# Kernel optimization log

Hardware: AMD Instinct MI355X
Metric: run time of the kernel (lower is better)

Reference implementation:

```python
import jax, jax.numpy as jnp
import numpy as np
from jax import lax

DIM = 64
HEADS = 2
BATCH, H, W = 4, 192, 192


def _conv1x1(x, w, b=None):
    # x: [b,c,h,w], w: [o,c]
    y = jnp.einsum('bchw,oc->bohw', x, w)
    if b is not None:
        y = y + b[None, :, None, None]
    return y


def _gelu(x):
    return jax.nn.gelu(x, approximate=False)  # torch nn.GELU default (erf)


def setup_inputs() -> dict:
    key = jax.random.key(0)
    ks = jax.random.split(key, 25)
    C = DIM
    n = lambda k, s, scale=0.05: jax.random.normal(k, s, dtype=jnp.float32) * scale
    return {
        'x': jax.random.normal(ks[0], (BATCH, C, H, W), dtype=jnp.float32),
        # BSConvU: pointwise (no bias) + depthwise 3x3 (bias)
        'pw_w': n(ks[1], (C, C)),
        'dw_w': n(ks[2], (C, 1, 3, 3)),
        'dw_b': n(ks[3], (C,)),
        'conv2_w': n(ks[4], (C, C)), 'conv2_b': n(ks[5], (C,)),
        'conv0_w': n(ks[6], (C, C)), 'conv0_b': n(ks[7], (C,)),
        # SelfAttention (bias=False)
        'att_q_w': n(ks[8], (C, C)), 'att_k_w': n(ks[9], (C, C)),
        'att_v_w': n(ks[10], (C, C)), 'att_proj_w': n(ks[11], (C, C)),
        'temperature': jnp.ones((HEADS, 1, 1), dtype=jnp.float32),
        # RowAttention (bias=False)
        'row_q_w': n(ks[12], (C, C)), 'row_k_w': n(ks[13], (C, C)),
        'row_v_w': n(ks[14], (C, C)),
        'row_gamma': n(ks[15], (1,), 0.5),
        # ColAttention (bias=False)
        'col_q_w': n(ks[16], (C, C)), 'col_k_w': n(ks[17], (C, C)),
        'col_v_w': n(ks[18], (C, C)),
        'col_gamma': n(ks[19], (1,), 0.5),
        # final fuse conv: in=3C, out=C
        'conv_w': n(ks[20], (C, 3 * C)), 'conv_b': n(ks[21], (C,)),
    }


def reference(x, pw_w, dw_w, dw_b, conv2_w, conv2_b, conv0_w, conv0_b,
              att_q_w, att_k_w, att_v_w, att_proj_w, temperature,
              row_q_w, row_k_w, row_v_w, row_gamma,
              col_q_w, col_k_w, col_v_w, col_gamma,
              conv_w, conv_b):
    b, c, h, w = x.shape
    # --- BSConvU -> GELU -> conv_2, plus conv_0 skip ---
    t = _conv1x1(x, pw_w)
    t = lax.conv_general_dilated(
        t, dw_w, window_strides=(1, 1), padding=((1, 1), (1, 1)),
        feature_group_count=c,
        dimension_numbers=('NCHW', 'OIHW', 'NCHW')) + dw_b[None, :, None, None]
    x1 = _conv1x1(_gelu(t), conv2_w, conv2_b) + _conv1x1(x, conv0_w, conv0_b)

    # --- channel self-attention (out_1) ---
    ch = c // HEADS
    q = _conv1x1(x1, att_q_w).reshape(b, HEADS, ch, h * w)
    k = _conv1x1(x1, att_k_w).reshape(b, HEADS, ch, h * w)
    v = _conv1x1(x1, att_v_w).reshape(b, HEADS, ch, h * w)
    q = q / jnp.maximum(jnp.linalg.norm(q, axis=-1, keepdims=True), 1e-12)
    k = k / jnp.maximum(jnp.linalg.norm(k, axis=-1, keepdims=True), 1e-12)
    attn = jnp.einsum('bgcn,bgdn->bgcd', q, k) * temperature[None]
    attn = jax.nn.softmax(attn, axis=-1)
    out1 = jnp.einsum('bgcd,bgdn->bgcn', attn, v).reshape(b, c, h, w)
    out1 = _conv1x1(out1, att_proj_w)

    # --- row attention over width, per (batch,row) (out_2) ---
    Q = _conv1x1(x1, row_q_w)
    K = _conv1x1(x1, row_k_w)
    V = _conv1x1(out1, row_v_w)
    s = jnp.einsum('bchi,bchj->bhij', Q, K)         # [b,h,w,w]
    a = jax.nn.softmax(s, axis=-1)
    out2 = jnp.einsum('bchj,bhij->bchi', V, a)
    out2 = row_gamma * out2 + x1

    # --- col attention over height, per (batch,col) (out_3) ---
    Q = _conv1x1(x1, col_q_w)
    K = _conv1x1(x1, col_k_w)
    V = _conv1x1(out1, col_v_w)
    s = jnp.einsum('bciw,bcjw->bwij', Q, K)         # [b,w,h,h]
    a = jax.nn.softmax(s, axis=-1)
    out3 = jnp.einsum('bcjw,bwij->bciw', V, a)
    out3 = col_gamma * out3 + x1

    out = jnp.concatenate([out1, out2, out3], axis=1)
    return _gelu(_conv1x1(out, conv_w, conv_b))
```

## Files before the change

kernel.cpp:

```cpp
#include <hip/hip_runtime.h>
#include <hip/hip_fp16.h>
#include <cstdio>

#define BB 4
#define C 64
#define HH 192
#define WW 192
#define NPIX (HH*WW)
#define ST (BB*C*NPIX)

__device__ __forceinline__ float gelu_f(float v) {
    return 0.5f * v * (1.0f + erff(v * 0.70710678118654752440f));
}

template<bool TWO_IN, bool PERB, bool DO_GELU>
__global__ __launch_bounds__(256, 3) void k_gconv(
    const float* __restrict__ in1, const float* __restrict__ in2,
    const float* __restrict__ W1, const float* __restrict__ W2,
    const float* __restrict__ bias1, const float* __restrict__ bias2,
    float* __restrict__ out, int ldw1, int ldw2)
{
    extern __shared__ float sm[];
    float* Wl = sm;
    float* Xl = sm + 4352;
    const int t = threadIdx.x;
    const int px0 = blockIdx.x * 128;
    const int b = blockIdx.y;
    const size_t base = (size_t)b*(C*NPIX) + px0;
    const int to = t >> 5, tp = t & 31;
    const int o0 = to*8, p0 = tp*4;
    float acc[8][4];
#pragma unroll
    for (int k = 0; k < 8; ++k) {
        float bo = 0.f;
        if (bias1) bo += bias1[o0+k];
        if (bias2) bo += bias2[o0+k];
#pragma unroll
        for (int m = 0; m < 4; ++m) acc[k][m] = bo;
    }
    const int NIN = TWO_IN ? 2 : 1;
#pragma unroll
    for (int inp = 0; inp < NIN; ++inp) {
        const float* In = inp ? in2 : in1;
        const float* Wk = inp ? W2 : (PERB ? W1 + b*4096 : W1);
        const int ldw = inp ? ldw2 : ldw1;
#pragma unroll
        for (int k = 0; k < 16; ++k) {
            const int idx = k*256 + t;
            const int o = idx >> 6, c = idx & 63;
            Wl[c*68 + o] = Wk[o*ldw + c];
        }
#pragma unroll
        for (int k = 0; k < 8; ++k) {
            const int f4 = k*256 + t;
            const int c = f4 >> 5, p4 = (f4 & 31)*4;
            *reinterpret_cast<float4*>(&Xl[c*132 + p4]) =
                *reinterpret_cast<const float4*>(&In[base + (size_t)c*NPIX + p4]);
        }
        __syncthreads();
#pragma unroll 2
        for (int c = 0; c < 64; ++c) {
            const float4 wa = *reinterpret_cast<const float4*>(&Wl[c*68 + o0]);
            const float4 wb = *reinterpret_cast<const float4*>(&Wl[c*68 + o0 + 4]);
            const float4 xv = *reinterpret_cast<const float4*>(&Xl[c*132 + p0]);
            const float wr[8] = {wa.x,wa.y,wa.z,wa.w, wb.x,wb.y,wb.z,wb.w};
            const float xr[4] = {xv.x,xv.y,xv.z,xv.w};
#pragma unroll
            for (int k = 0; k < 8; ++k)
#pragma unroll
                for (int m = 0; m < 4; ++m) acc[k][m] += wr[k]*xr[m];
        }
        __syncthreads();
    }
#pragma unroll
    for (int k = 0; k < 8; ++k) {
        float4 o4;
        if (DO_GELU) {
            o4.x = gelu_f(acc[k][0]); o4.y = gelu_f(acc[k][1]);
            o4.z = gelu_f(acc[k][2]); o4.w = gelu_f(acc[k][3]);
        } else {
            o4.x = acc[k][0]; o4.y = acc[k][1];
            o4.z = acc[k][2]; o4.w = acc[k][3];
        }
        *reinterpret_cast<float4*>(&out[base + (size_t)(o0+k)*NPIX + p0]) = o4;
    }
}

__global__ __launch_bounds__(256, 3) void k_conv4(
    const float* __restrict__ i1, const float* __restrict__ i2,
    const float* __restrict__ i3, const float* __restrict__ i4,
    const float* __restrict__ W1, const float* __restrict__ W2,
    const float* __restrict__ W3, const float* __restrict__ W4,
    const float* __restrict__ bias, float* __restrict__ out)
{
    extern __shared__ float sm[];
    float* Wl = sm;
    float* Xl = sm + 4352;
    const int t = threadIdx.x;
    const int px0 = blockIdx.x * 128;
    const int b = blockIdx.y;
    const size_t base = (size_t)b*(C*NPIX) + px0;
    const int to = t >> 5, tp = t & 31;
    const int o0 = to*8, p0 = tp*4;
    float acc[8][4];
#pragma unroll
    for (int k = 0; k < 8; ++k) {
        const float bo = bias[o0+k];
#pragma unroll
        for (int m = 0; m < 4; ++m) acc[k][m] = bo;
    }
#pragma unroll
    for (int inp = 0; inp < 4; ++inp) {
        const float* In = (inp==0)?i1:(inp==1)?i2:(inp==2)?i3:i4;
        const float* Wk = (inp==0)?W1:(inp==1)?W2:(inp==2)?W3:W4;
        const int ldw = (inp==0)?192:64;
#pragma unroll
        for (int k = 0; k < 16; ++k) {
            const int idx = k*256 + t;
            const int o = idx >> 6, c = idx & 63;
            Wl[c*68 + o] = Wk[o*ldw + c];
        }
#pragma unroll
        for (int k = 0; k < 8; ++k) {
            const int f4 = k*256 + t;
            const int c = f4 >> 5, p4 = (f4 & 31)*4;
            *reinterpret_cast<float4*>(&Xl[c*132 + p4]) =
                *reinterpret_cast<const float4*>(&In[base + (size_t)c*NPIX + p4]);
        }
        __syncthreads();
#pragma unroll 2
        for (int c = 0; c < 64; ++c) {
            const float4 wa = *reinterpret_cast<const float4*>(&Wl[c*68 + o0]);
            const float4 wb = *reinterpret_cast<const float4*>(&Wl[c*68 + o0 + 4]);
            const float4 xv = *reinterpret_cast<const float4*>(&Xl[c*132 + p0]);
            const float wr[8] = {wa.x,wa.y,wa.z,wa.w, wb.x,wb.y,wb.z,wb.w};
            const float xr[4] = {xv.x,xv.y,xv.z,xv.w};
#pragma unroll
            for (int k = 0; k < 8; ++k)
#pragma unroll
                for (int m = 0; m < 4; ++m) acc[k][m] += wr[k]*xr[m];
        }
        __syncthreads();
    }
#pragma unroll
    for (int k = 0; k < 8; ++k) {
        float4 o4;
        o4.x = gelu_f(acc[k][0]); o4.y = gelu_f(acc[k][1]);
        o4.z = gelu_f(acc[k][2]); o4.w = gelu_f(acc[k][3]);
        *reinterpret_cast<float4*>(&out[base + (size_t)(o0+k)*NPIX + p0]) = o4;
    }
}

__global__ __launch_bounds__(192) void k_dw(
    const float* __restrict__ t0, const float* __restrict__ w,
    const float* __restrict__ bias, float* __restrict__ g)
{
    const int x = threadIdx.x;
    const int y = blockIdx.x;
    const int bc = blockIdx.y;
    const int c = bc & 63;
    const float* img = t0 + bc * NPIX;
    const float* wc = w + c * 9;
    float acc = bias[c];
#pragma unroll
    for (int dy = -1; dy <= 1; ++dy) {
        const int yy = y + dy;
        if (yy < 0 || yy > 191) continue;
#pragma unroll
        for (int dx = -1; dx <= 1; ++dx) {
            const int xx = x + dx;
            if (xx < 0 || xx > 191) continue;
            acc += img[yy*WW + xx] * wc[(dy+1)*3 + (dx+1)];
        }
    }
    g[bc*NPIX + y*WW + x] = gelu_f(acc);
}

__global__ __launch_bounds__(256) void k_gram_part(
    const float* __restrict__ x1p, float* __restrict__ part)
{
    extern __shared__ float lt[];
    const int chunk = blockIdx.x, b = blockIdx.y, t = threadIdx.x;
    const int gbase = b * (C*NPIX) + chunk * 256;
    for (int idx = t; idx < C*256; idx += 256) {
        const int c = idx >> 8, n = idx & 255;
        lt[n*68 + c] = x1p[gbase + c*NPIX + n];
    }
    __syncthreads();
    const int ti = t & 15, tj = t >> 4;
    float acc[4][4];
#pragma unroll
    for (int r = 0; r < 4; ++r)
#pragma unroll
        for (int s = 0; s < 4; ++s) acc[r][s] = 0.f;
    for (int n = 0; n < 256; ++n) {
        const float4 av = *reinterpret_cast<const float4*>(&lt[n*68 + 4*ti]);
        const float4 bv = *reinterpret_cast<const float4*>(&lt[n*68 + 4*tj]);
        const float ar[4] = {av.x, av.y, av.z, av.w};
        const float br[4] = {bv.x, bv.y, bv.z, bv.w};
#pragma unroll
        for (int r = 0; r < 4; ++r)
#pragma unroll
            for (int s = 0; s < 4; ++s) acc[r][s] += ar[r] * br[s];
    }
    float* pb = part + (b*144 + chunk)*4096;
#pragma unroll
    for (int r = 0; r < 4; ++r)
#pragma unroll
        for (int s = 0; s < 4; ++s) pb[(4*ti+r)*64 + (4*tj+s)] = acc[r][s];
}

__global__ __launch_bounds__(256) void k_gram_reduce(
    const float* __restrict__ part, float* __restrict__ G1)
{
    const int flat = blockIdx.x*256 + threadIdx.x;
    const int b = flat >> 12, ij = flat & 4095;
    float s = 0.f;
    for (int ch = 0; ch < 144; ++ch) s += part[(b*144+ch)*4096 + ij];
    G1[flat] = s;
}

__global__ __launch_bounds__(256) void k_attn_small(
    const float* __restrict__ G1a, const float* __restrict__ Wq,
    const float* __restrict__ Wk, const float* __restrict__ Wv,
    const float* __restrict__ Wp, const float* __restrict__ temp,
    float* __restrict__ M2)
{
    extern __shared__ float sm[];
    float* g1 = sm;
    float* wa = sm + 4096;
    float* wb = sm + 8192;
    float* u  = sm + 12288;
    float* at = sm + 16384;
    float* nq = sm + 18432;
    float* nk = sm + 18496;
    const int b = blockIdx.x, t = threadIdx.x;
    const float* G = G1a + b*4096;
    for (int i = t; i < 4096; i += 256) { g1[i] = G[i]; wa[i] = Wq[i]; wb[i] = Wk[i]; }
    __syncthreads();
    {
        const int r = t >> 2, q4 = t & 3;
        for (int cc = q4*16; cc < q4*16 + 16; ++cc) {
            float s = 0.f;
            for (int k = 0; k < 64; ++k) s += wa[r*64+k] * g1[k*64+cc];
            u[r*64+cc] = s;
        }
    }
    __syncthreads();
    {
        const int d = t >> 2, kq = t & 3;
        float p = 0.f;
        for (int k = kq*16; k < kq*16 + 16; ++k) {
            float tk = 0.f;
            for (int c2 = 0; c2 < 64; ++c2) tk += g1[k*64+c2] * wb[d*64+c2];
            p += wb[d*64+k] * tk;
        }
        p += __shfl_xor(p, 1);
        p += __shfl_xor(p, 2);
        if (kq == 0) nk[d] = sqrtf(fmaxf(p, 0.f));
    }
    if (t < 64) {
        float s = 0.f;
        for (int c2 = 0; c2 < 64; ++c2) s += u[t*64+c2] * wa[t*64+c2];
        nq[t] = sqrtf(fmaxf(s, 0.f));
    }
    __syncthreads();
    if (t < 64) {
        const int gI = t >> 5;
        const float tg = temp[gI];
        const float dq = fmaxf(nq[t], 1e-12f);
        float row[32];
        float mx = -1e30f;
#pragma unroll
        for (int d2 = 0; d2 < 32; ++d2) {
            const int dd = gI*32 + d2;
            float s = 0.f;
            for (int c2 = 0; c2 < 64; ++c2) s += u[t*64+c2] * wb[dd*64+c2];
            s = s * tg / (dq * fmaxf(nk[dd], 1e-12f));
            row[d2] = s; mx = fmaxf(mx, s);
        }
        float se = 0.f;
#pragma unroll
        for (int d2 = 0; d2 < 32; ++d2) { row[d2] = __expf(row[d2]-mx); se += row[d2]; }
        const float inv = 1.f / se;
#pragma unroll
        for (int d2 = 0; d2 < 32; ++d2) at[t*32+d2] = row[d2]*inv;
    }
    __syncthreads();
    for (int i = t; i < 4096; i += 256) { wa[i] = Wv[i]; wb[i] = Wp[i]; }
    __syncthreads();
    {
        const int m = t >> 2, q4 = t & 3, gI = m >> 5;
        for (int e = q4*16; e < q4*16 + 16; ++e) {
            float s = 0.f;
#pragma unroll
            for (int d2 = 0; d2 < 32; ++d2) s += at[m*32+d2] * wa[(gI*32+d2)*64 + e];
            g1[m*64+e] = s;
        }
    }
    __syncthreads();
    {
        const int o = t >> 2, q4 = t & 3;
        for (int e = q4*16; e < q4*16 + 16; ++e) {
            float s = 0.f;
            for (int m = 0; m < 64; ++m) s += wb[o*64+m] * g1[m*64+e];
            M2[b*4096 + o*64+e] = s;
        }
    }
}

__global__ __launch_bounds__(256) void k_small_mats(
    const float* __restrict__ rq, const float* __restrict__ rk,
    const float* __restrict__ cq, const float* __restrict__ ck,
    const float* __restrict__ fw, const float* __restrict__ rv,
    const float* __restrict__ cv, const float* __restrict__ rg,
    const float* __restrict__ cg,
    float* __restrict__ Wtr, float* __restrict__ Wtc,
    float* __restrict__ Wf2p, float* __restrict__ Wf3p,
    float* __restrict__ Wfx)
{
    const int which = blockIdx.x, t = threadIdx.x;
    const int a = t >> 2, b0 = (t & 3) * 16;
    if (which <= 1) {
        const float* Q = which ? cq : rq;
        const float* Kw = which ? ck : rk;
        float* O = which ? Wtc : Wtr;
        for (int b = b0; b < b0 + 16; ++b) {
            float s = 0.f;
            for (int co = 0; co < 64; ++co) s += Q[co*64 + a] * Kw[co*64 + b];
            O[a*64 + b] = s;
        }
    } else if (which <= 3) {
        const float* Vw = (which == 2) ? rv : cv;
        const float g = (which == 2) ? rg[0] : cg[0];
        const int off = (which == 2) ? 64 : 128;
        float* O = (which == 2) ? Wf2p : Wf3p;
        for (int b = b0; b < b0 + 16; ++b) {
            float s = 0.f;
            for (int m = 0; m < 64; ++m) s += fw[a*192 + off + m] * Vw[m*64 + b];
            O[a*64 + b] = g * s;
        }
    } else {
        for (int b = b0; b < b0 + 16; ++b)
            Wfx[a*64 + b] = fw[a*192 + 64 + b] + fw[a*192 + 128 + b];
    }
}

#define SP 196
__global__ __launch_bounds__(256, 2) void k_attn_fused(
    const float* __restrict__ X, const float* __restrict__ Wt,
    const float* __restrict__ U, float* __restrict__ Z)
{
    extern __shared__ float sm[];
    float* Xl = sm;
    __half* Ylh = reinterpret_cast<__half*>(sm + 12544);
    __half* Plh = reinterpret_cast<__half*>(sm);
    float* red  = sm;
    float* mrow = sm + 3264;
    float* lrow = sm + 18816;
    const int t = threadIdx.x;
    const int h = blockIdx.x, b = blockIdx.y;
    const size_t gbase = (size_t)b*(C*NPIX) + (size_t)h*WW;

#pragma unroll 4
    for (int k = 0; k < 48; ++k) {
        const int idx = k*256 + t;
        const int c = idx / 192, j = idx - c*192;
        Xl[c*SP + j] = X[gbase + (size_t)c*NPIX + j];
    }
    __syncthreads();

    {
        const int tc = t & 15, tjy = t >> 4;
        const int c0 = 4*tc, j0y = 12*tjy;
        float accy[4][12];
#pragma unroll
        for (int k = 0; k < 4; ++k)
#pragma unroll
            for (int m = 0; m < 12; ++m) accy[k][m] = 0.f;
        for (int a = 0; a < 64; ++a) {
            const float4 w4 = *reinterpret_cast<const float4*>(&Wt[a*64 + c0]);
            const float4 xa = *reinterpret_cast<const float4*>(&Xl[a*SP + j0y]);
            const float4 xb = *reinterpret_cast<const float4*>(&Xl[a*SP + j0y + 4]);
            const float4 xc = *reinterpret_cast<const float4*>(&Xl[a*SP + j0y + 8]);
            const float wr[4]  = {w4.x, w4.y, w4.z, w4.w};
            const float xr[12] = {xa.x,xa.y,xa.z,xa.w, xb.x,xb.y,xb.z,xb.w,
                                  xc.x,xc.y,xc.z,xc.w};
#pragma unroll
            for (int k = 0; k < 4; ++k)
#pragma unroll
                for (int m = 0; m < 12; ++m) accy[k][m] += wr[k] * xr[m];
        }
#pragma unroll
        for (int k = 0; k < 4; ++k) {
            __half2* yr = reinterpret_cast<__half2*>(&Ylh[(c0+k)*SP + j0y]);
#pragma unroll
            for (int q = 0; q < 6; ++q)
                yr[q] = __floats2half2_rn(accy[k][2*q], accy[k][2*q+1]);
        }
    }
    __syncthreads();

    const int ti = t & 15, tj = t >> 4;
    const int i0 = ti*12, j0 = tj*12;
    float acc[12][12];
#pragma unroll
    for (int r = 0; r < 12; ++r)
#pragma unroll
        for (int s = 0; s < 12; ++s) acc[r][s] = 0.f;
#pragma unroll 2
    for (int c = 0; c < 64; ++c) {
        const float4 xa = *reinterpret_cast<const float4*>(&Xl[c*SP + i0]);
        const float4 xb = *reinterpret_cast<const float4*>(&Xl[c*SP + i0 + 4]);
        const float4 xc = *reinterpret_cast<const float4*>(&Xl[c*SP + i0 + 8]);
        const __half2* yp = reinterpret_cast<const __half2*>(&Ylh[c*SP + j0]);
        const float2 y0 = __half22float2(yp[0]);
        const float2 y1 = __half22float2(yp[1]);
        const float2 y2 = __half22float2(yp[2]);
        const float2 y3 = __half22float2(yp[3]);
        const float2 y4 = __half22float2(yp[4]);
        const float2 y5 = __half22float2(yp[5]);
        const float xr[12] = {xa.x,xa.y,xa.z,xa.w, xb.x,xb.y,xb.z,xb.w, xc.x,xc.y,xc.z,xc.w};
        const float yr[12] = {y0.x,y0.y, y1.x,y1.y, y2.x,y2.y,
                              y3.x,y3.y, y4.x,y4.y, y5.x,y5.y};
#pragma unroll
        for (int r = 0; r < 12; ++r)
#pragma unroll
            for (int s = 0; s < 12; ++s) acc[r][s] += xr[r] * yr[s];
    }
    __syncthreads();

#pragma unroll
    for (int r = 0; r < 12; ++r) {
        float pm = acc[r][0];
#pragma unroll
        for (int s = 1; s < 12; ++s) pm = fmaxf(pm, acc[r][s]);
        red[(i0 + r)*17 + tj] = pm;
    }
    __syncthreads();
    if (t < 192) {
        float m = red[t*17];
#pragma unroll
        for (int k = 1; k < 16; ++k) m = fmaxf(m, red[t*17 + k]);
        mrow[t] = m;
    }
    __syncthreads();
#pragma unroll
    for (int r = 0; r < 12; ++r) {
        const float mi = mrow[i0 + r];
        float ps = 0.f;
#pragma unroll
        for (int s = 0; s < 12; ++s) {
            acc[r][s] = __expf(acc[r][s] - mi);
            ps += acc[r][s];
        }
        red[(i0 + r)*17 + tj] = ps;
    }
    __syncthreads();
    if (t < 192) {
        float l = 0.f;
#pragma unroll
        for (int k = 0; k < 16; ++k) l += red[t*17 + k];
        lrow[t] = 1.f / l;
    }
    __syncthreads();

#pragma unroll
    for (int r = 0; r < 12; ++r) {
        __half2* pr = reinterpret_cast<__half2*>(&Plh[(i0 + r)*SP + j0]);
#pragma unroll
        for (int q = 0; q < 6; ++q)
            pr[q] = __floats2half2_rn(acc[r][2*q], acc[r][2*q+1]);
    }
    __syncthreads();

    const int ci = t & 15, ii = t >> 4;
    const int c0z = 4*ci, i0z = 12*ii;
    const float* Ub = U + gbase;
    float accz[4][12];
#pragma unroll
    for (int k = 0; k < 4; ++k)
#pragma unroll
        for (int m = 0; m < 12; ++m) accz[k][m] = 0.f;
#pragma unroll 2
    for (int jq = 0; jq < 48; ++jq) {
        const int j4 = 4*jq;
        float4 u4[4];
#pragma unroll
        for (int k = 0; k < 4; ++k)
            u4[k] = *reinterpret_cast<const float4*>(&Ub[(size_t)(c0z+k)*NPIX + j4]);
        float2 pa[12], pb[12];
#pragma unroll
        for (int m = 0; m < 12; ++m) {
            const __half2* pp = reinterpret_cast<const __half2*>(&Plh[(i0z+m)*SP + j4]);
            pa[m] = __half22float2(pp[0]);
            pb[m] = __half22float2(pp[1]);
        }
#pragma unroll
        for (int k = 0; k < 4; ++k)
#pragma unroll
            for (int m = 0; m < 12; ++m) {
                accz[k][m] += u4[k].x * pa[m].x + u4[k].y * pa[m].y
                            + u4[k].z * pb[m].x + u4[k].w * pb[m].y;
            }
    }
    float lr[12];
#pragma unroll
    for (int m = 0; m < 12; ++m) lr[m] = lrow[i0z + m];
#pragma unroll
    for (int k = 0; k < 4; ++k) {
        float* zr = Z + gbase + (size_t)(c0z + k)*NPIX + i0z;
        float4 o0, o1, o2;
        o0.x = accz[k][0]*lr[0]; o0.y = accz[k][1]*lr[1];  o0.z = accz[k][2]*lr[2];   o0.w = accz[k][3]*lr[3];
        o1.x = accz[k][4]*lr[4]; o1.y = accz[k][5]*lr[5];  o1.z = accz[k][6]*lr[6];   o1.w = accz[k][7]*lr[7];
        o2.x = accz[k][8]*lr[8]; o2.y = accz[k][9]*lr[9];  o2.z = accz[k][10]*lr[10]; o2.w = accz[k][11]*lr[11];
        *reinterpret_cast<float4*>(zr)     = o0;
        *reinterpret_cast<float4*>(zr + 4) = o1;
        *reinterpret_cast<float4*>(zr + 8) = o2;
    }
}

__global__ __launch_bounds__(256) void k_transpose(
    const float* __restrict__ in, float* __restrict__ out)
{
    __shared__ float tile[32][33];
    const int tx = threadIdx.x & 31, ty = threadIdx.x >> 5;
    const int x0 = blockIdx.x*32, y0 = blockIdx.y*32;
    const float* img = in + blockIdx.z * NPIX;
    float* og = out + blockIdx.z * NPIX;
#pragma unroll
    for (int r = ty; r < 32; r += 8) tile[r][tx] = img[(y0+r)*WW + x0+tx];
    __syncthreads();
#pragma unroll
    for (int r = ty; r < 32; r += 8) og[(x0+r)*WW + (y0+tx)] = tile[tx][r];
}

__global__ __launch_bounds__(256) void k_transpose2(
    const float* __restrict__ inA, float* __restrict__ outA,
    const float* __restrict__ inB, float* __restrict__ outB)
{
    __shared__ float tile[32][33];
    const int tx = threadIdx.x & 31, ty = threadIdx.x >> 5;
    const int x0 = blockIdx.x*32, y0 = blockIdx.y*32;
    const int z = blockIdx.z;
    const float* img = (z < BB*C) ? inA + (size_t)z*NPIX
                                  : inB + (size_t)(z - BB*C)*NPIX;
    float* og = (z < BB*C) ? outA + (size_t)z*NPIX
                           : outB + (size_t)(z - BB*C)*NPIX;
#pragma unroll
    for (int r = ty; r < 32; r += 8) tile[r][tx] = img[(y0+r)*WW + x0+tx];
    __syncthreads();
#pragma unroll
    for (int r = ty; r < 32; r += 8) og[(x0+r)*WW + (y0+tx)] = tile[tx][r];
}

extern "C" void kernel_launch(void* const* d_in, const int* in_sizes, int n_in,
                              void* d_out, int out_size, void* d_ws, size_t ws_size,
                              hipStream_t stream) {
    const float* x       = (const float*)d_in[0];
    const float* pw_w    = (const float*)d_in[1];
    const float* dw_w    = (const float*)d_in[2];
    const float* dw_b    = (const float*)d_in[3];
    const float* conv2_w = (const float*)d_in[4];
    const float* conv2_b = (const float*)d_in[5];
    const float* conv0_w = (const float*)d_in[6];
    const float* conv0_b = (const float*)d_in[7];
    const float* attq    = (const float*)d_in[8];
    const float* attk    = (const float*)d_in[9];
    const float* attv    = (const float*)d_in[10];
    const float* attp    = (const float*)d_in[11];
    const float* temp    = (const float*)d_in[12];
    const float* rq      = (const float*)d_in[13];
    const float* rk      = (const float*)d_in[14];
    const float* rv      = (const float*)d_in[15];
    const float* rg      = (const float*)d_in[16];
    const float* cq      = (const float*)d_in[17];
    const float* ck      = (const float*)d_in[18];
    const float* cv      = (const float*)d_in[19];
    const float* cg      = (const float*)d_in[20];
    const float* fw      = (const float*)d_in[21];
    const float* fb      = (const float*)d_in[22];

    float* ws = (float*)d_ws;
    float* A  = ws;
    float* Bf = ws + (size_t)ST;
    float* Cf = ws + 2*(size_t)ST;
    float* Df = ws + 3*(size_t)ST;
    float* Ef = ws + 4*(size_t)ST;
    float* partials = ws + 5*(size_t)ST;
    float* G1 = partials + 576*4096;
    float* M2 = G1 + 16384;
    float* Wtr  = M2 + 16384;
    float* Wtc  = Wtr + 4096;
    float* Wf2p = Wtc + 4096;
    float* Wf3p = Wf2p + 4096;
    float* Wfx  = Wf3p + 4096;

    const size_t need = ((size_t)5*ST + 576*4096 + 16384 + 16384 + 5*4096)
                        * sizeof(float);
    if (ws_size < need) {
        fprintf(stderr, "kernel_launch: ws_size %zu < needed %zu\n", ws_size, need);
        return;
    }

    (void)hipFuncSetAttribute((const void*)k_gram_part,
        hipFuncAttributeMaxDynamicSharedMemorySize, 69632);
    (void)hipFuncSetAttribute((const void*)k_attn_small,
        hipFuncAttributeMaxDynamicSharedMemorySize, 74240);
    (void)hipFuncSetAttribute((const void*)k_attn_fused,
        hipFuncAttributeMaxDynamicSharedMemorySize, 76032);
    (void)hipFuncSetAttribute((const void*)k_conv4,
        hipFuncAttributeMaxDynamicSharedMemorySize, 51200);
    (void)hipFuncSetAttribute((const void*)(k_gconv<false,false,false>),
        hipFuncAttributeMaxDynamicSharedMemorySize, 51200);
    (void)hipFuncSetAttribute((const void*)(k_gconv<true,false,false>),
        hipFuncAttributeMaxDynamicSharedMemorySize, 51200);
    (void)hipFuncSetAttribute((const void*)(k_gconv<false,true,false>),
        hipFuncAttributeMaxDynamicSharedMemorySize, 51200);

    const dim3 blk256(256), blk192(192);
    const dim3 gconv(NPIX/128, BB);
    const dim3 ggram(NPIX/256, BB);
    const dim3 gline(HH, BB);
    const dim3 gtr(6, 6, BB*C);
    const dim3 gtr2(6, 6, 2*BB*C);

    k_small_mats<<<dim3(5), blk256, 0, stream>>>(rq, rk, cq, ck, fw, rv, cv,
                                                 rg, cg, Wtr, Wtc, Wf2p, Wf3p, Wfx);
    k_gconv<false,false,false><<<gconv, blk256, 51200, stream>>>(
        x, nullptr, pw_w, nullptr, nullptr, nullptr, A, 64, 64);
    k_dw<<<dim3(HH, BB*C), blk192, 0, stream>>>(A, dw_w, dw_b, Bf);
    k_gconv<true,false,false><<<gconv, blk256, 51200, stream>>>(
        Bf, x, conv2_w, conv0_w, conv2_b, conv0_b, A, 64, 64);
    k_gram_part<<<ggram, blk256, 69632, stream>>>(A, partials);
    k_gram_reduce<<<dim3(64), blk256, 0, stream>>>(partials, G1);
    k_attn_small<<<dim3(BB), blk256, 74240, stream>>>(G1, attq, attk, attv, attp, temp, M2);
    k_gconv<false,true,false><<<gconv, blk256, 51200, stream>>>(
        A, nullptr, M2, nullptr, nullptr, nullptr, Bf, 64, 64);
    k_transpose2<<<gtr2, blk256, 0, stream>>>(A, Cf, Bf, Df);
    k_attn_fused<<<gline, blk256, 76032, stream>>>(Cf, Wtc, Df, Ef);
    k_transpose<<<gtr, blk256, 0, stream>>>(Ef, Df);
    k_attn_fused<<<gline, blk256, 76032, stream>>>(A, Wtr, Bf, Cf);
    k_conv4<<<gconv, blk256, 51200, stream>>>(
        Bf, Cf, Df, A, fw, Wf2p, Wf3p, Wfx, fb, (float*)d_out);
}
```

Before: 841.2 us.

## Use packed fp16 dot2 instructions in fused row/column attention matmuls

Stores X, Y, P and U as packed half2 with channel pairs interleaved, and replaces the scalar fp32 FMA inner loops of the three attention matmuls with v_dot2 fp16 accumulate-to-fp32 instructions. Each dot2 does two multiply-adds, so the ALU work in the Q·K score, projection and P·V stages should roughly halve, and shared-memory footprint per element shrinks. In exchange, X, the projection weights and V are now rounded to fp16 with round-toward-zero conversion (previously X and V stayed fp32), which lowers accuracy, and the layout change increases shared memory slightly.

```diff
diff --git a/kernel.cpp b/kernel.cpp
--- a/kernel.cpp
+++ b/kernel.cpp
@@ -1,5 +1,4 @@
 #include <hip/hip_runtime.h>
-#include <hip/hip_fp16.h>
 #include <cstdio>
 
 #define BB 4
@@ -11,6 +10,32 @@
 
 __device__ __forceinline__ float gelu_f(float v) {
     return 0.5f * v * (1.0f + erff(v * 0.70710678118654752440f));
+}
+
+typedef __fp16 h2 __attribute__((ext_vector_type(2)));
+
+__device__ __forceinline__ h2 pkh2(float lo, float hi) {
+#if __has_builtin(__builtin_amdgcn_cvt_pkrtz)
+    return __builtin_amdgcn_cvt_pkrtz(lo, hi);
+#else
+    h2 r; r[0] = (__fp16)lo; r[1] = (__fp16)hi; return r;
+#endif
+}
+
+__device__ __forceinline__ float dot2f(h2 a, h2 b, float c) {
+#if __has_builtin(__builtin_amdgcn_fdot2)
+    return __builtin_amdgcn_fdot2(a, b, c, false);
+#else
+    return c + (float)a[0]*(float)b[0] + (float)a[1]*(float)b[1];
+#endif
+}
+
+__device__ __forceinline__ void ld4h2(const void* p, h2* d) {
+    const float4 f = *reinterpret_cast<const float4*>(p);
+    d[0] = __builtin_bit_cast(h2, f.x);
+    d[1] = __builtin_bit_cast(h2, f.y);
+    d[2] = __builtin_bit_cast(h2, f.z);
+    d[3] = __builtin_bit_cast(h2, f.w);
 }
 
 template<bool TWO_IN, bool PERB, bool DO_GELU>
@@ -347,26 +372,29 @@
 }
 
 #define SP 196
+#define PSTR 100
 __global__ __launch_bounds__(256, 2) void k_attn_fused(
     const float* __restrict__ X, const float* __restrict__ Wt,
     const float* __restrict__ U, float* __restrict__ Z)
 {
     extern __shared__ float sm[];
-    float* Xl = sm;
-    __half* Ylh = reinterpret_cast<__half*>(sm + 12544);
-    __half* Plh = reinterpret_cast<__half*>(sm);
+    h2* Xh = reinterpret_cast<h2*>(sm);
+    h2* Yh = reinterpret_cast<h2*>(sm + 6272);
+    h2* Ph = reinterpret_cast<h2*>(sm);
     float* red  = sm;
     float* mrow = sm + 3264;
-    float* lrow = sm + 18816;
+    float* lrow = sm + 19200;
     const int t = threadIdx.x;
     const int h = blockIdx.x, b = blockIdx.y;
     const size_t gbase = (size_t)b*(C*NPIX) + (size_t)h*WW;
 
 #pragma unroll 4
-    for (int k = 0; k < 48; ++k) {
+    for (int k = 0; k < 24; ++k) {
         const int idx = k*256 + t;
-        const int c = idx / 192, j = idx - c*192;
-        Xl[c*SP + j] = X[gbase + (size_t)c*NPIX + j];
+        const int cc = idx / 192, j = idx - cc*192;
+        const float lo = X[gbase + (size_t)(2*cc)*NPIX + j];
+        const float hi = X[gbase + (size_t)(2*cc+1)*NPIX + j];
+        Xh[cc*SP + j] = pkh2(lo, hi);
     }
     __syncthreads();
 
@@ -378,25 +406,26 @@
         for (int k = 0; k < 4; ++k)
 #pragma unroll
             for (int m = 0; m < 12; ++m) accy[k][m] = 0.f;
-        for (int a = 0; a < 64; ++a) {
-            const float4 w4 = *reinterpret_cast<const float4*>(&Wt[a*64 + c0]);
-            const float4 xa = *reinterpret_cast<const float4*>(&Xl[a*SP + j0y]);
-            const float4 xb = *reinterpret_cast<const float4*>(&Xl[a*SP + j0y + 4]);
-            const float4 xc = *reinterpret_cast<const float4*>(&Xl[a*SP + j0y + 8]);
-            const float wr[4]  = {w4.x, w4.y, w4.z, w4.w};
-            const float xr[12] = {xa.x,xa.y,xa.z,xa.w, xb.x,xb.y,xb.z,xb.w,
-                                  xc.x,xc.y,xc.z,xc.w};
+        for (int aa = 0; aa < 32; ++aa) {
+            const float4 wlo = *reinterpret_cast<const float4*>(&Wt[(2*aa)*64 + c0]);
+            const float4 whi = *reinterpret_cast<const float4*>(&Wt[(2*aa+1)*64 + c0]);
+            h2 wh[4];
+            wh[0] = pkh2(wlo.x, whi.x); wh[1] = pkh2(wlo.y, whi.y);
+            wh[2] = pkh2(wlo.z, whi.z); wh[3] = pkh2(wlo.w, whi.w);
+            h2 xh[12];
+            ld4h2(&Xh[aa*SP + j0y],     xh);
+            ld4h2(&Xh[aa*SP + j0y + 4], xh+4);
+            ld4h2(&Xh[aa*SP + j0y + 8], xh+8);
 #pragma unroll
             for (int k = 0; k < 4; ++k)
 #pragma unroll
-                for (int m = 0; m < 12; ++m) accy[k][m] += wr[k] * xr[m];
-        }
-#pragma unroll
-        for (int k = 0; k < 4; ++k) {
-            __half2* yr = reinterpret_cast<__half2*>(&Ylh[(c0+k)*SP + j0y]);
-#pragma unroll
-            for (int q = 0; q < 6; ++q)
-                yr[q] = __floats2half2_rn(accy[k][2*q], accy[k][2*q+1]);
+                for (int m = 0; m < 12; ++m)
+                    accy[k][m] = dot2f(wh[k], xh[m], accy[k][m]);
+        }
+#pragma unroll
+        for (int m = 0; m < 12; ++m) {
+            Yh[(2*tc)*SP + j0y + m]   = pkh2(accy[0][m], accy[1][m]);
+            Yh[(2*tc+1)*SP + j0y + m] = pkh2(accy[2][m], accy[3][m]);
         }
     }
     __syncthreads();
@@ -409,24 +438,19 @@
 #pragma unroll
         for (int s = 0; s < 12; ++s) acc[r][s] = 0.f;
 #pragma unroll 2
-    for (int c = 0; c < 64; ++c) {
-        const float4 xa = *reinterpret_cast<const float4*>(&Xl[c*SP + i0]);
-        const float4 xb = *reinterpret_cast<const float4*>(&Xl[c*SP + i0 + 4]);
-        const float4 xc = *reinterpret_cast<const float4*>(&Xl[c*SP + i0 + 8]);
-        const __half2* yp = reinterpret_cast<const __half2*>(&Ylh[c*SP + j0]);
-        const float2 y0 = __half22float2(yp[0]);
-        const float2 y1 = __half22float2(yp[1]);
-        const float2 y2 = __half22float2(yp[2]);
-        const float2 y3 = __half22float2(yp[3]);
-        const float2 y4 = __half22float2(yp[4]);
-        const float2 y5 = __half22float2(yp[5]);
-        const float xr[12] = {xa.x,xa.y,xa.z,xa.w, xb.x,xb.y,xb.z,xb.w, xc.x,xc.y,xc.z,xc.w};
-        const float yr[12] = {y0.x,y0.y, y1.x,y1.y, y2.x,y2.y,
-                              y3.x,y3.y, y4.x,y4.y, y5.x,y5.y};
+    for (int cc = 0; cc < 32; ++cc) {
+        h2 xh[12], yh[12];
+        ld4h2(&Xh[cc*SP + i0],     xh);
+        ld4h2(&Xh[cc*SP + i0 + 4], xh+4);
+        ld4h2(&Xh[cc*SP + i0 + 8], xh+8);
+        ld4h2(&Yh[cc*SP + j0],     yh);
+        ld4h2(&Yh[cc*SP + j0 + 4], yh+4);
+        ld4h2(&Yh[cc*SP + j0 + 8], yh+8);
 #pragma unroll
         for (int r = 0; r < 12; ++r)
 #pragma unroll
-            for (int s = 0; s < 12; ++s) acc[r][s] += xr[r] * yr[s];
+            for (int s = 0; s < 12; ++s)
+                acc[r][s] = dot2f(xh[r], yh[s], acc[r][s]);
     }
     __syncthreads();
 
@@ -465,12 +489,13 @@
     }
     __syncthreads();
 
-#pragma unroll
-    for (int r = 0; r < 12; ++r) {
-        __half2* pr = reinterpret_cast<__half2*>(&Plh[(i0 + r)*SP + j0]);
-#pragma unroll
-        for (int q = 0; q < 6; ++q)
-            pr[q] = __floats2half2_rn(acc[r][2*q], acc[r][2*q+1]);
+    {
+        const int jh0 = j0 >> 1;
+#pragma unroll
+        for (int r = 0; r < 12; ++r)
+#pragma unroll
+            for (int q = 0; q < 6; ++q)
+                Ph[(i0 + r)*PSTR + jh0 + q] = pkh2(acc[r][2*q], acc[r][2*q+1]);
     }
     __syncthreads();
 
@@ -482,26 +507,29 @@
     for (int k = 0; k < 4; ++k)
 #pragma unroll
         for (int m = 0; m < 12; ++m) accz[k][m] = 0.f;
-#pragma unroll 2
-    for (int jq = 0; jq < 48; ++jq) {
-        const int j4 = 4*jq;
-        float4 u4[4];
+    for (int jt = 0; jt < 192; jt += 8) {
+        h2 uh[4][4];
+#pragma unroll
+        for (int k = 0; k < 4; ++k) {
+            const float4 ua = *reinterpret_cast<const float4*>(&Ub[(size_t)(c0z+k)*NPIX + jt]);
+            const float4 ub = *reinterpret_cast<const float4*>(&Ub[(size_t)(c0z+k)*NPIX + jt + 4]);
+            uh[k][0] = pkh2(ua.x, ua.y); uh[k][1] = pkh2(ua.z, ua.w);
+            uh[k][2] = pkh2(ub.x, ub.y); uh[k][3] = pkh2(ub.z, ub.w);
+        }
+        h2 ph[12][4];
+#pragma unroll
+        for (int m = 0; m < 12; ++m)
+            ld4h2(&Ph[(i0z+m)*PSTR + (jt >> 1)], ph[m]);
 #pragma unroll
         for (int k = 0; k < 4; ++k)
-            u4[k] = *reinterpret_cast<const float4*>(&Ub[(size_t)(c0z+k)*NPIX + j4]);
-        float2 pa[12], pb[12];
-#pragma unroll
-        for (int m = 0; m < 12; ++m) {
-            const __half2* pp = reinterpret_cast<const __half2*>(&Plh[(i0z+m)*SP + j4]);
-            pa[m] = __half22float2(pp[0]);
-            pb[m] = __half22float2(pp[1]);
-        }
-#pragma unroll
-        for (int k = 0; k < 4; ++k)
 #pragma unroll
             for (int m = 0; m < 12; ++m) {
-                accz[k][m] += u4[k].x * pa[m].x + u4[k].y * pa[m].y
-                            + u4[k].z * pb[m].x + u4[k].w * pb[m].y;
+                float a = accz[k][m];
+                a = dot2f(uh[k][0], ph[m][0], a);
+                a = dot2f(uh[k][1], ph[m][1], a);
+                a = dot2f(uh[k][2], ph[m][2], a);
+                a = dot2f(uh[k][3], ph[m][3], a);
+                accz[k][m] = a;
             }
     }
     float lr[12];
@@ -608,7 +636,7 @@
     (void)hipFuncSetAttribute((const void*)k_attn_small,
         hipFuncAttributeMaxDynamicSharedMemorySize, 74240);
     (void)hipFuncSetAttribute((const void*)k_attn_fused,
-        hipFuncAttributeMaxDynamicSharedMemorySize, 76032);
+        hipFuncAttributeMaxDynamicSharedMemorySize, 77568);
     (void)hipFuncSetAttribute((const void*)k_conv4,
         hipFuncAttributeMaxDynamicSharedMemorySize, 51200);
     (void)hipFuncSetAttribute((const void*)(k_gconv<false,false,false>),
@@ -638,9 +666,9 @@
     k_gconv<false,true,false><<<gconv, blk256, 51200, stream>>>(
         A, nullptr, M2, nullptr, nullptr, nullptr, Bf, 64, 64);
     k_transpose2<<<gtr2, blk256, 0, stream>>>(A, Cf, Bf, Df);
-    k_attn_fused<<<gline, blk256, 76032, stream>>>(Cf, Wtc, Df, Ef);
+    k_attn_fused<<<gline, blk256, 77568, stream>>>(Cf, Wtc, Df, Ef);
     k_transpose<<<gtr, blk256, 0, stream>>>(Ef, Df);
-    k_attn_fused<<<gline, blk256, 76032, stream>>>(A, Wtr, Bf, Cf);
+    k_attn_fused<<<gline, blk256, 77568, stream>>>(A, Wtr, Bf, Cf);
     k_conv4<<<gconv, blk256, 51200, stream>>>(
         Bf, Cf, Df, A, fw, Wf2p, Wf3p, Wfx, fb, (float*)d_out);
 }
```

After: 810.3 us. 3.7% less time.
